# Optimization experiments

Measured on AMD Instinct MI355X. Metric: run time of the kernel, lower is better.

The kernel has to match this reference:

```python
import jax, jax.numpy as jnp
import numpy as np

B, N, D = 32, 2048, 1024


def setup_inputs() -> dict:
    key = jax.random.key(0)
    k1, k2, k3, k4, k5, k6 = jax.random.split(key, 6)
    encoded = jax.random.normal(k1, (B, N, D), dtype=jnp.float32)
    decoder_state = jax.random.normal(k2, (B, D), dtype=jnp.float32)
    mask = jax.random.randint(k3, (B, N), 0, 2, dtype=jnp.int32)
    scale = 1.0 / np.sqrt(D)
    W1 = jax.random.normal(k4, (D, D), dtype=jnp.float32) * scale  # applied as x @ W1
    W2 = jax.random.normal(k5, (D, D), dtype=jnp.float32) * scale
    vt = jax.random.normal(k6, (D,), dtype=jnp.float32) * scale
    return {"encoded": encoded, "decoder_state": decoder_state, "mask": mask,
            "W1": W1, "W2": W2, "vt": vt}


def reference(encoded, decoder_state, mask, W1, W2, vt):
    temperature = 1.0
    # process_encoded: W1(encoded)  [B, N, D]
    enc = jnp.einsum('bnd,de->bne', encoded, W1)
    # W2(decoder_state)  [B, D] -> broadcast-add over N
    dec = decoder_state @ W2
    # vt(tanh(.)).squeeze(2)  -> logits [B, N]
    u = jnp.einsum('bnd,d->bn', jnp.tanh(enc + dec[:, None, :]), vt)
    # masked log-softmax with temperature over dim=1
    logits = u / temperature + jnp.log(mask.astype(u.dtype) + 1e-45)
    return jax.nn.log_softmax(logits, axis=1)
```

## Files before the change

### kernel.cpp

```cpp
#include <hip/hip_runtime.h>

typedef _Float16 half8 __attribute__((ext_vector_type(8)));
typedef _Float16 half4 __attribute__((ext_vector_type(4)));
typedef __fp16   pk2   __attribute__((ext_vector_type(2)));
typedef float    f32x4 __attribute__((ext_vector_type(4)));

#define GLOBAL_AS __attribute__((address_space(1)))
#define LDS_AS    __attribute__((address_space(3)))

static constexpr int Bb = 32;
static constexpr int Nn = 2048;
static constexpr int Dd = 1024;
static constexpr int M  = Bb * Nn;


__global__ void prep_w1(const float* __restrict__ W1, _Float16* __restrict__ W1TT) {
    int g = blockIdx.x * 256 + threadIdx.x;
    int chunk = g >> 10;
    int u = g & 1023;
    int q = u >> 7, sc = u & 127;
    int cl = sc ^ (2 * (q & 3));
    int et = chunk >> 5, t = (chunk >> 1) & 15, h = chunk & 1;
    int e  = et * 256 + h * 128 + cl;
    int k0 = t * 64 + q * 8;
    half8 hh;
#pragma unroll
    for (int j = 0; j < 8; ++j)
        hh[j] = (_Float16)W1[(size_t)(k0 + j) * Dd + e];
    *(half8*)(W1TT + (size_t)g * 8) = hh;
}

__global__ void dec_kernel(const float* __restrict__ ds, const float* __restrict__ W2,
                           float* __restrict__ dec) {
    __shared__ float part[4][64];
    int b = blockIdx.x, ech = blockIdx.y;
    int tid = threadIdx.x;
    int e = ech * 64 + (tid & 63);
    int dc = tid >> 6;
    float acc = 0.f;
#pragma unroll 4
    for (int d = dc * 256; d < dc * 256 + 256; ++d)
        acc += ds[b * Dd + d] * W2[(size_t)d * Dd + e];
    part[dc][tid & 63] = acc;
    __syncthreads();
    if (tid < 64)
        dec[b * Dd + e] = part[0][tid] + part[1][tid] + part[2][tid] + part[3][tid];
}

#define BAR     asm volatile("s_barrier" ::: "memory")
#define LGKM(n) asm volatile("s_waitcnt lgkmcnt(" #n ")" ::: "memory")
#define VM(n)   asm volatile("s_waitcnt vmcnt(" #n ")" ::: "memory")
#define PRIO1   __builtin_amdgcn_s_setprio(1)
#define PRIO0   __builtin_amdgcn_s_setprio(0)

#define RD_A(dst, base) do { _Pragma("unroll") \
  for (int ks = 0; ks < 2; ++ks) { \
    _Pragma("unroll") for (int m2 = 0; m2 < 4; ++m2) { \
      const int row_ = m2 * 32 + rA; \
      const int kc0_ = (ks * 4 + qq) * 2; \
      dst[m2][ks] = *(const half8*)&lds[(base) + (row_ * 16 + (kc0_ ^ rxa)) * 4]; \
    } } } while (0)

#define RD_B(dst, base) do { _Pragma("unroll") \
  for (int ks = 0; ks < 2; ++ks) { const int qb = ((ks * 4 + qq) * 128) * 8; \
    _Pragma("unroll") for (int j2 = 0; j2 < 2; ++j2) \
      dst[j2][ks] = *(const half8*)&lds[(base) + qb + (j2 * 64 + rB) * 8]; } } while (0)

#define MFMAQ(A_, B_, ro, co) do { \
  _Pragma("unroll") for (int m2 = 0; m2 < 4; ++m2) \
  _Pragma("unroll") for (int j2 = 0; j2 < 2; ++j2) { \
    acc[(ro) + m2][(co) + j2] = __builtin_amdgcn_mfma_f32_16x16x32_f16( \
        A_[m2][0], B_[j2][0], acc[(ro) + m2][(co) + j2], 0, 0, 0); \
    acc[(ro) + m2][(co) + j2] = __builtin_amdgcn_mfma_f32_16x16x32_f16( \
        A_[m2][1], B_[j2][1], acc[(ro) + m2][(co) + j2], 0, 0, 0); } } while (0)

__global__ __launch_bounds__(512, 2) void gemm8(
    const float* __restrict__ encA, const _Float16* __restrict__ W1TT,
    const float* __restrict__ dec, const float* __restrict__ vt,
    float* __restrict__ u_part)
{
    extern __shared__ _Float16 lds[];

    const int g  = blockIdx.x;
    const int wg = (g & 7) * 128 + (g >> 3);
    const int et    = wg & 3;
    const int mtile = wg >> 2;

    const int tid  = threadIdx.x;
    const int lane = tid & 63, wid = tid >> 6;
    const int wr = wid >> 2, wc = wid & 3;
    const int qq = lane >> 4, l15 = lane & 15;
    const int l15s = l15 ^ (2 * qq);
    const int rA = wr * 16 + l15;
    const int rxa = (l15 & 7) * 2;
    const int rB = wc * 16 + l15s;

    f32x4 acc[8][4] = {};
    half8 a[4][2], b0[2][2], b1[2][2];
    f32x4 aSt[4];

    const int arow0 = tid >> 4;
    const int l16   = tid & 15;
    const float* agp = encA + (((size_t)(mtile * 256 + arow0)) << 10) + l16 * 4;

    const size_t bbase = (size_t)et * 32 * 8192;
    const int uoff = tid * 8;

    auto issueA = [&](int T, int h) {
        const float* gp = agp + T * 64 + ((size_t)h << 17);
#pragma unroll
        for (int p = 0; p < 4; ++p)
            aSt[p] = *(const f32x4*)(gp + ((size_t)p << 15));
    };
    auto writeA = [&](int Tn, int h) {
        const int base = ((Tn & 1) << 14) + h * 8192;
#pragma unroll
        for (int p = 0; p < 4; ++p) {
            const int row = p * 32 + arow0;
            pk2 c0 = __builtin_amdgcn_cvt_pkrtz(aSt[p][0], aSt[p][1]);
            pk2 c1 = __builtin_amdgcn_cvt_pkrtz(aSt[p][2], aSt[p][3]);
            half4 hh; hh[0] = c0[0]; hh[1] = c0[1]; hh[2] = c1[0]; hh[3] = c1[1];
            *(half4*)&lds[base + (row * 16 + (l16 ^ ((row & 7) * 2))) * 4] = hh;
        }
    };
    auto stB = [&](int T, int h) {
        const _Float16* gp = W1TT + bbase + ((size_t)(T * 2 + h) << 13) + uoff;
        _Float16* lp = lds + (32768 + (((T & 1) * 2 + h) << 13) + (wid << 9));
        __builtin_amdgcn_global_load_lds((const GLOBAL_AS void*)gp,
                                         (LDS_AS void*)lp, 16, 0, 0);
        __builtin_amdgcn_global_load_lds((const GLOBAL_AS void*)(gp + 4096),
                                         (LDS_AS void*)(lp + 4096), 16, 0, 0);
    };


    issueA(0, 0); stB(0, 0); stB(0, 1);
    VM(4);  writeA(0, 0);
    __builtin_amdgcn_sched_barrier(0);
    issueA(0, 1);
    VM(0);  writeA(0, 1);
    LGKM(0);
    BAR;

#pragma unroll 1
    for (int T = 0; T < 16; ++T) {
        const int As  = (T & 1) << 14;
        const int Bs2 = 32768 + ((T & 1) << 14);
        const bool s = (T < 15);

        if (s) { issueA(T + 1, 0); stB(T + 1, 0); stB(T + 1, 1); }

        RD_A(a, As);
        RD_B(b0, Bs2);
        RD_B(b1, Bs2 + 8192);
        LGKM(4);
        PRIO1; MFMAQ(a, b0, 0, 0); PRIO0;
        LGKM(0);
        PRIO1; MFMAQ(a, b1, 0, 2); PRIO0;
        RD_A(a, As + 8192);
        if (s) {
            VM(4);
            writeA(T + 1, 0);
            __builtin_amdgcn_sched_barrier(0);
            issueA(T + 1, 1);
            LGKM(4);
        } else {
            LGKM(0);
        }
        PRIO1; MFMAQ(a, b0, 4, 0); MFMAQ(a, b1, 4, 2); PRIO0;

        VM(0);
        if (s) writeA(T + 1, 1);
        LGKM(0);
        BAR;
    }

    const int b = mtile >> 3;
    float vtv[4], dcv[4];
#pragma unroll
    for (int nf = 0; nf < 4; ++nf) {
        int e = et * 256 + (nf >> 1) * 128 + (nf & 1) * 64 + wc * 16 + l15;
        vtv[nf] = vt[e];
        dcv[nf] = dec[b * Dd + e];
    }
    float* usum = (float*)lds;
#pragma unroll
    for (int hm = 0; hm < 8; ++hm) {
        const int h = hm >> 2, mq = hm & 3;
#pragma unroll
        for (int r = 0; r < 4; ++r) {
            float sv = 0.f;
#pragma unroll
            for (int nf = 0; nf < 4; ++nf) {
                float x  = acc[hm][nf][r] + dcv[nf];
                float ex = __expf(2.f * x);
                sv += (1.f - 2.f * __builtin_amdgcn_rcpf(ex + 1.f)) * vtv[nf];
            }
#pragma unroll
            for (int off = 1; off < 16; off <<= 1) sv += __shfl_xor(sv, off, 16);
            if (l15 == 0)
                usum[wc * 256 + h * 128 + mq * 32 + wr * 16 + qq * 4 + r] = sv;
        }
    }
    __syncthreads();
    if (tid < 256) {
        float v = usum[tid] + usum[256 + tid] + usum[512 + tid] + usum[768 + tid];
        u_part[(size_t)et * M + (size_t)mtile * 256 + tid] = v;
    }
}

__global__ void softmax_k(const float* __restrict__ up, const int* __restrict__ mask,
                          float* __restrict__ out) {
    __shared__ float red[8];
    int b = blockIdx.x, tid = threadIdx.x;
    float l[8];
#pragma unroll
    for (int i = 0; i < 8; ++i) {
        int n = i * 256 + tid;
        float s = up[(size_t)b * Nn + n];
#pragma unroll
        for (int et = 1; et < 4; ++et) s += up[(size_t)et * M + (size_t)b * Nn + n];
        l[i] = s + (mask[b * Nn + n] ? 0.f : -103.278931f);
    }
    float m = l[0];
#pragma unroll
    for (int i = 1; i < 8; ++i) m = fmaxf(m, l[i]);
#pragma unroll
    for (int o = 32; o >= 1; o >>= 1) m = fmaxf(m, __shfl_xor(m, o, 64));
    if ((tid & 63) == 0) red[tid >> 6] = m;
    __syncthreads();
    m = fmaxf(fmaxf(red[0], red[1]), fmaxf(red[2], red[3]));
    float s = 0.f;
#pragma unroll
    for (int i = 0; i < 8; ++i) s += expf(l[i] - m);
#pragma unroll
    for (int o = 32; o >= 1; o >>= 1) s += __shfl_xor(s, o, 64);
    if ((tid & 63) == 0) red[4 + (tid >> 6)] = s;
    __syncthreads();
    float lse = m + logf(red[4] + red[5] + red[6] + red[7]);
#pragma unroll
    for (int i = 0; i < 8; ++i)
        out[(size_t)b * Nn + i * 256 + tid] = l[i] - lse;
}

extern "C" void kernel_launch(void* const* d_in, const int* in_sizes, int n_in,
                              void* d_out, int out_size, void* d_ws, size_t ws_size,
                              hipStream_t stream) {
    const float* encoded = (const float*)d_in[0];
    const float* dstate  = (const float*)d_in[1];
    const int*   mask    = (const int*)d_in[2];
    const float* W1      = (const float*)d_in[3];
    const float* W2      = (const float*)d_in[4];
    const float* vt      = (const float*)d_in[5];
    float* out = (float*)d_out;

    char* ws = (char*)d_ws;
    float*    u_part = (float*)ws;
    float*    dec    = (float*)(ws + (size_t)4 * M * 4);
    _Float16* W1TT   = (_Float16*)(ws + (size_t)4 * M * 4 + (size_t)Bb * Dd * 4);

    static bool attr_done = false;
    if (!attr_done) {
        hipFuncSetAttribute(reinterpret_cast<const void*>(gemm8),
                            hipFuncAttributeMaxDynamicSharedMemorySize, 131072);
        attr_done = true;
    }

    prep_w1<<<512, 256, 0, stream>>>(W1, W1TT);
    dec_kernel<<<dim3(32, 16), 256, 0, stream>>>(dstate, W2, dec);
    gemm8<<<1024, 512, 131072, stream>>>(encoded, W1TT, dec, vt, u_part);
    softmax_k<<<32, 256, 0, stream>>>(u_part, mask, out);
}
```

Baseline: 541.5 us.

## Use 4-wave GEMM with 128x128 per-wave tiles and merge prep kernels

Rewrites the main GEMM from 8 waves with 64x64 per-wave tiles to 4 waves (256 threads), each computing a 128x128 tile with an 8x8 MFMA accumulator. The aim is to raise LDS-fragment reuse per MFMA and cut the LDS read traffic per FLOP. It also fuses the W1 conversion and decoder-state GEMV kernels into one launch to save a launch. The risk is much higher register pressure (256 accumulator VGPRs plus fragments) and fewer waves per CU, which reduces latency hiding for the global loads.

```diff
diff --git a/kernel.cpp b/kernel.cpp
--- a/kernel.cpp
+++ b/kernel.cpp
@@ -14,37 +14,41 @@
 static constexpr int M  = Bb * Nn;
 
 
-__global__ void prep_w1(const float* __restrict__ W1, _Float16* __restrict__ W1TT) {
-    int g = blockIdx.x * 256 + threadIdx.x;
-    int chunk = g >> 10;
-    int u = g & 1023;
-    int q = u >> 7, sc = u & 127;
-    int cl = sc ^ (2 * (q & 3));
-    int et = chunk >> 5, t = (chunk >> 1) & 15, h = chunk & 1;
-    int e  = et * 256 + h * 128 + cl;
-    int k0 = t * 64 + q * 8;
-    half8 hh;
-#pragma unroll
-    for (int j = 0; j < 8; ++j)
-        hh[j] = (_Float16)W1[(size_t)(k0 + j) * Dd + e];
-    *(half8*)(W1TT + (size_t)g * 8) = hh;
-}
-
-__global__ void dec_kernel(const float* __restrict__ ds, const float* __restrict__ W2,
-                           float* __restrict__ dec) {
-    __shared__ float part[4][64];
-    int b = blockIdx.x, ech = blockIdx.y;
-    int tid = threadIdx.x;
-    int e = ech * 64 + (tid & 63);
-    int dc = tid >> 6;
-    float acc = 0.f;
+__global__ void prep0(const float* __restrict__ W1, _Float16* __restrict__ W1TT,
+                      const float* __restrict__ ds, const float* __restrict__ W2,
+                      float* __restrict__ dec) {
+    const int id = blockIdx.x;
+    const int tid = threadIdx.x;
+    if (id < 512) {
+        int g = id * 256 + tid;
+        int chunk = g >> 10;
+        int u = g & 1023;
+        int q = u >> 7, sc = u & 127;
+        int cl = sc ^ (2 * (q & 3));
+        int et = chunk >> 5, t = (chunk >> 1) & 15, h = chunk & 1;
+        int e  = et * 256 + h * 128 + cl;
+        int k0 = t * 64 + q * 8;
+        half8 hh;
+#pragma unroll
+        for (int j = 0; j < 8; ++j)
+            hh[j] = (_Float16)W1[(size_t)(k0 + j) * Dd + e];
+        *(half8*)(W1TT + (size_t)g * 8) = hh;
+    } else {
+        __shared__ float part[4][64];
+        const int id2 = id - 512;
+        const int b = id2 >> 4, ech = id2 & 15;
+        int e = ech * 64 + (tid & 63);
+        int dc = tid >> 6;
+        float acc = 0.f;
 #pragma unroll 4
-    for (int d = dc * 256; d < dc * 256 + 256; ++d)
-        acc += ds[b * Dd + d] * W2[(size_t)d * Dd + e];
-    part[dc][tid & 63] = acc;
-    __syncthreads();
-    if (tid < 64)
-        dec[b * Dd + e] = part[0][tid] + part[1][tid] + part[2][tid] + part[3][tid];
+        for (int d = dc * 256; d < dc * 256 + 256; ++d)
+            acc += ds[b * Dd + d] * W2[(size_t)d * Dd + e];
+        part[dc][tid & 63] = acc;
+        __syncthreads();
+        if (tid < 64)
+            dec[b * Dd + e] = part[0][tid] + part[1][tid]
+                            + part[2][tid] + part[3][tid];
+    }
 }
 
 #define BAR     asm volatile("s_barrier" ::: "memory")
@@ -53,28 +57,27 @@
 #define PRIO1   __builtin_amdgcn_s_setprio(1)
 #define PRIO0   __builtin_amdgcn_s_setprio(0)
 
-#define RD_A(dst, base) do { _Pragma("unroll") \
-  for (int ks = 0; ks < 2; ++ks) { \
-    _Pragma("unroll") for (int m2 = 0; m2 < 4; ++m2) { \
-      const int row_ = m2 * 32 + rA; \
-      const int kc0_ = (ks * 4 + qq) * 2; \
-      dst[m2][ks] = *(const half8*)&lds[(base) + (row_ * 16 + (kc0_ ^ rxa)) * 4]; \
-    } } } while (0)
-
-#define RD_B(dst, base) do { _Pragma("unroll") \
-  for (int ks = 0; ks < 2; ++ks) { const int qb = ((ks * 4 + qq) * 128) * 8; \
-    _Pragma("unroll") for (int j2 = 0; j2 < 2; ++j2) \
-      dst[j2][ks] = *(const half8*)&lds[(base) + qb + (j2 * 64 + rB) * 8]; } } while (0)
-
-#define MFMAQ(A_, B_, ro, co) do { \
-  _Pragma("unroll") for (int m2 = 0; m2 < 4; ++m2) \
-  _Pragma("unroll") for (int j2 = 0; j2 < 2; ++j2) { \
-    acc[(ro) + m2][(co) + j2] = __builtin_amdgcn_mfma_f32_16x16x32_f16( \
-        A_[m2][0], B_[j2][0], acc[(ro) + m2][(co) + j2], 0, 0, 0); \
-    acc[(ro) + m2][(co) + j2] = __builtin_amdgcn_mfma_f32_16x16x32_f16( \
-        A_[m2][1], B_[j2][1], acc[(ro) + m2][(co) + j2], 0, 0, 0); } } while (0)
-
-__global__ __launch_bounds__(512, 2) void gemm8(
+#define RD_A(ks_) do { _Pragma("unroll") \
+  for (int m_ = 0; m_ < 8; ++m_) { \
+    const int row_ = wrbase + m_ * 16 + l15; \
+    a[m_][ks_] = *(const half8*)&lds[As + row_ * 64 \
+                    + ((((ks_) * 4 + qq) * 2) ^ rxa) * 4]; \
+  } } while (0)
+
+#define RD_B(ks_) do { _Pragma("unroll") \
+  for (int n_ = 0; n_ < 8; ++n_) \
+    b[n_][ks_] = *(const half8*)&lds[Bs + wcoff \
+                    + ((((ks_) * 4 + qq) * 128) + n_ * 16 + l15x) * 8]; \
+  } while (0)
+
+#define PASS(ks_) do { _Pragma("unroll") \
+  for (int m_ = 0; m_ < 8; ++m_) \
+  _Pragma("unroll") for (int n_ = 0; n_ < 8; ++n_) \
+    acc[m_][n_] = __builtin_amdgcn_mfma_f32_16x16x32_f16( \
+        a[m_][ks_], b[n_][ks_], acc[m_][n_], 0, 0, 0); \
+  } while (0)
+
+__global__ __launch_bounds__(256, 1) void gemm4(
     const float* __restrict__ encA, const _Float16* __restrict__ W1TT,
     const float* __restrict__ dec, const float* __restrict__ vt,
     float* __restrict__ u_part)
@@ -88,54 +91,53 @@
 
     const int tid  = threadIdx.x;
     const int lane = tid & 63, wid = tid >> 6;
-    const int wr = wid >> 2, wc = wid & 3;
+    const int wr = wid >> 1, wc = wid & 1;
     const int qq = lane >> 4, l15 = lane & 15;
-    const int l15s = l15 ^ (2 * qq);
-    const int rA = wr * 16 + l15;
-    const int rxa = (l15 & 7) * 2;
-    const int rB = wc * 16 + l15s;
-
-    f32x4 acc[8][4] = {};
-    half8 a[4][2], b0[2][2], b1[2][2];
-    f32x4 aSt[4];
+    const int rxa   = (l15 & 7) * 2;
+    const int l15x  = l15 ^ (2 * qq);
+    const int wrbase = wr * 128;
+    const int wcoff  = wc * 8192;
+
+    f32x4 acc[8][8] = {};
+    half8 a[8][2], b[8][2];
+    f32x4 aSt[8];
 
     const int arow0 = tid >> 4;
     const int l16   = tid & 15;
     const float* agp = encA + (((size_t)(mtile * 256 + arow0)) << 10) + l16 * 4;
 
     const size_t bbase = (size_t)et * 32 * 8192;
-    const int uoff = tid * 8;
 
     auto issueA = [&](int T, int h) {
         const float* gp = agp + T * 64 + ((size_t)h << 17);
 #pragma unroll
-        for (int p = 0; p < 4; ++p)
-            aSt[p] = *(const f32x4*)(gp + ((size_t)p << 15));
+        for (int p = 0; p < 8; ++p)
+            aSt[p] = *(const f32x4*)(gp + ((size_t)p << 14));
     };
     auto writeA = [&](int Tn, int h) {
-        const int base = ((Tn & 1) << 14) + h * 8192;
-#pragma unroll
-        for (int p = 0; p < 4; ++p) {
-            const int row = p * 32 + arow0;
+        const int slot = (Tn & 1) << 14;
+#pragma unroll
+        for (int p = 0; p < 8; ++p) {
+            const int row = h * 128 + p * 16 + arow0;
             pk2 c0 = __builtin_amdgcn_cvt_pkrtz(aSt[p][0], aSt[p][1]);
             pk2 c1 = __builtin_amdgcn_cvt_pkrtz(aSt[p][2], aSt[p][3]);
             half4 hh; hh[0] = c0[0]; hh[1] = c0[1]; hh[2] = c1[0]; hh[3] = c1[1];
-            *(half4*)&lds[base + (row * 16 + (l16 ^ ((row & 7) * 2))) * 4] = hh;
+            *(half4*)&lds[slot + row * 64 + (l16 ^ (2 * (arow0 & 7))) * 4] = hh;
         }
     };
-    auto stB = [&](int T, int h) {
-        const _Float16* gp = W1TT + bbase + ((size_t)(T * 2 + h) << 13) + uoff;
-        _Float16* lp = lds + (32768 + (((T & 1) * 2 + h) << 13) + (wid << 9));
-        __builtin_amdgcn_global_load_lds((const GLOBAL_AS void*)gp,
-                                         (LDS_AS void*)lp, 16, 0, 0);
-        __builtin_amdgcn_global_load_lds((const GLOBAL_AS void*)(gp + 4096),
-                                         (LDS_AS void*)(lp + 4096), 16, 0, 0);
+    auto stB = [&](int T) {
+        const _Float16* gp0 = W1TT + bbase + (((size_t)T * 2) << 13);
+        _Float16* lp0 = lds + 32768 + ((T & 1) << 14);
+#pragma unroll
+        for (int c = 0; c < 8; ++c)
+            __builtin_amdgcn_global_load_lds(
+                (const GLOBAL_AS void*)(gp0 + (size_t)(c * 256 + tid) * 8),
+                (LDS_AS void*)(lp0 + (c * 256 + wid * 64) * 8), 16, 0, 0);
     };
 
 
-    issueA(0, 0); stB(0, 0); stB(0, 1);
-    VM(4);  writeA(0, 0);
-    __builtin_amdgcn_sched_barrier(0);
+    issueA(0, 0); stB(0);
+    VM(8);  writeA(0, 0);
     issueA(0, 1);
     VM(0);  writeA(0, 1);
     LGKM(0);
@@ -143,69 +145,63 @@
 
 #pragma unroll 1
     for (int T = 0; T < 16; ++T) {
-        const int As  = (T & 1) << 14;
-        const int Bs2 = 32768 + ((T & 1) << 14);
+        const int As = (T & 1) << 14;
+        const int Bs = 32768 + ((T & 1) << 14);
         const bool s = (T < 15);
 
-        if (s) { issueA(T + 1, 0); stB(T + 1, 0); stB(T + 1, 1); }
-
-        RD_A(a, As);
-        RD_B(b0, Bs2);
-        RD_B(b1, Bs2 + 8192);
-        LGKM(4);
-        PRIO1; MFMAQ(a, b0, 0, 0); PRIO0;
-        LGKM(0);
-        PRIO1; MFMAQ(a, b1, 0, 2); PRIO0;
-        RD_A(a, As + 8192);
+        if (s) { issueA(T + 1, 0); stB(T + 1); }
+
+        RD_A(0);
+        RD_B(0);
+        RD_A(1);
+        LGKM(8);
+        RD_B(1);
+        PRIO1; PASS(0); PRIO0;
         if (s) {
-            VM(4);
+            VM(8);
             writeA(T + 1, 0);
-            __builtin_amdgcn_sched_barrier(0);
             issueA(T + 1, 1);
-            LGKM(4);
+            LGKM(8);
         } else {
             LGKM(0);
         }
-        PRIO1; MFMAQ(a, b0, 4, 0); MFMAQ(a, b1, 4, 2); PRIO0;
-
+        PRIO1; PASS(1); PRIO0;
         VM(0);
         if (s) writeA(T + 1, 1);
         LGKM(0);
         BAR;
     }
 
-    const int b = mtile >> 3;
-    float vtv[4], dcv[4];
-#pragma unroll
-    for (int nf = 0; nf < 4; ++nf) {
-        int e = et * 256 + (nf >> 1) * 128 + (nf & 1) * 64 + wc * 16 + l15;
-        vtv[nf] = vt[e];
-        dcv[nf] = dec[b * Dd + e];
+    const int bidx = mtile >> 3;
+    float vtv[8], dcv[8];
+#pragma unroll
+    for (int n = 0; n < 8; ++n) {
+        int e = et * 256 + wc * 128 + n * 16 + l15;
+        vtv[n] = vt[e];
+        dcv[n] = dec[bidx * Dd + e];
     }
     float* usum = (float*)lds;
 #pragma unroll
-    for (int hm = 0; hm < 8; ++hm) {
-        const int h = hm >> 2, mq = hm & 3;
+    for (int m = 0; m < 8; ++m) {
 #pragma unroll
         for (int r = 0; r < 4; ++r) {
             float sv = 0.f;
 #pragma unroll
-            for (int nf = 0; nf < 4; ++nf) {
-                float x  = acc[hm][nf][r] + dcv[nf];
+            for (int n = 0; n < 8; ++n) {
+                float x  = acc[m][n][r] + dcv[n];
                 float ex = __expf(2.f * x);
-                sv += (1.f - 2.f * __builtin_amdgcn_rcpf(ex + 1.f)) * vtv[nf];
+                sv += (1.f - 2.f * __builtin_amdgcn_rcpf(ex + 1.f)) * vtv[n];
             }
 #pragma unroll
             for (int off = 1; off < 16; off <<= 1) sv += __shfl_xor(sv, off, 16);
             if (l15 == 0)
-                usum[wc * 256 + h * 128 + mq * 32 + wr * 16 + qq * 4 + r] = sv;
+                usum[wc * 256 + wrbase + m * 16 + qq * 4 + r] = sv;
         }
     }
     __syncthreads();
-    if (tid < 256) {
-        float v = usum[tid] + usum[256 + tid] + usum[512 + tid] + usum[768 + tid];
-        u_part[(size_t)et * M + (size_t)mtile * 256 + tid] = v;
-    }
+    if (tid < 256)
+        u_part[(size_t)et * M + (size_t)mtile * 256 + tid]
+            = usum[tid] + usum[256 + tid];
 }
 
 __global__ void softmax_k(const float* __restrict__ up, const int* __restrict__ mask,
@@ -260,13 +256,12 @@
 
     static bool attr_done = false;
     if (!attr_done) {
-        hipFuncSetAttribute(reinterpret_cast<const void*>(gemm8),
+        hipFuncSetAttribute(reinterpret_cast<const void*>(gemm4),
                             hipFuncAttributeMaxDynamicSharedMemorySize, 131072);
         attr_done = true;
     }
 
-    prep_w1<<<512, 256, 0, stream>>>(W1, W1TT);
-    dec_kernel<<<dim3(32, 16), 256, 0, stream>>>(dstate, W2, dec);
-    gemm8<<<1024, 512, 131072, stream>>>(encoded, W1TT, dec, vt, u_part);
+    prep0<<<1024, 256, 0, stream>>>(W1, W1TT, dstate, W2, dec);
+    gemm4<<<1024, 256, 131072, stream>>>(encoded, W1TT, dec, vt, u_part);
     softmax_k<<<32, 256, 0, stream>>>(u_part, mask, out);
 }
```

After: 791.2 us. +46.1%, slower.
